# Kernel optimization log

Hardware: AMD Instinct MI355X
Metric: run time of the kernel (lower is better)

## Reference

```python
import jax, jax.numpy as jnp
import numpy as np

N_MELS = 80
FORMANT_START, FORMANT_END = 10, 50
W_L1, W_DELTA, W_DELTA2, W_SC, W_BAND, FORMANT_W = 1.0, 0.5, 0.25, 0.5, 1.0, 2.0
EPS = 1e-8


def _masked_mean(x, mask):
    # mask broadcasts to x's shape; count = sum of the broadcast mask
    n = jnp.maximum(jnp.sum(jnp.broadcast_to(mask, x.shape)), 1.0)
    return jnp.sum(x * mask) / n


def setup_inputs() -> dict:
    key = jax.random.key(0)
    k1, k2, k3 = jax.random.split(key, 3)
    B, T, D = 64, 4000, N_MELS
    pred_mel = jax.random.normal(k1, (B, T, D), dtype=jnp.float32)
    target_mel = jax.random.normal(k2, (B, T, D), dtype=jnp.float32)
    lengths = jax.random.randint(k3, (B,), T // 2, T + 1)
    mel_mask = (jnp.arange(T)[None, :] < lengths[:, None]).astype(jnp.float32)
    band_weights = jnp.ones((D,), dtype=jnp.float32).at[FORMANT_START:FORMANT_END].set(FORMANT_W)
    return {"pred_mel": pred_mel, "target_mel": target_mel, "mel_mask": mel_mask,
            "band_weights": band_weights}


def reference(pred_mel, target_mel, mel_mask, band_weights):
    mask3 = mel_mask[:, :, None]                      # (B,T,1)

    l1 = jnp.abs(pred_mel - target_mel)               # (B,T,D)
    l1_loss = _masked_mean(l1, mask3)

    # 1st-order deltas
    dp = pred_mel[:, 1:] - pred_mel[:, :-1]
    dt = target_mel[:, 1:] - target_mel[:, :-1]
    dmask = (mel_mask[:, 1:] * mel_mask[:, :-1])[:, :, None]
    delta_loss = _masked_mean(jnp.abs(dp - dt), dmask)

    # 2nd-order deltas
    d2p = dp[:, 1:] - dp[:, :-1]
    d2t = dt[:, 1:] - dt[:, :-1]
    d2mask = (mel_mask[:, 2:] * mel_mask[:, 1:-1] * mel_mask[:, :-2])[:, :, None]
    delta2_loss = _masked_mean(jnp.abs(d2p - d2t), d2mask)

    # spectral convergence
    diff = (pred_mel - target_mel) * mask3
    tgt_m = target_mel * mask3
    n = jnp.maximum(jnp.sum(jnp.broadcast_to(mask3, pred_mel.shape)), 1.0)
    sc_num = jnp.sqrt(jnp.sum(diff * diff) / n)
    sc_den = jnp.maximum(jnp.sqrt(jnp.sum(tgt_m * tgt_m) / n), EPS)
    sc_loss = sc_num / sc_den

    # band-weighted L1
    w = band_weights[None, None, :]
    band_loss = _masked_mean(l1 * w, mask3) / jnp.mean(band_weights)

    # energy (per-frame mean over mel bins)
    e_l1 = jnp.abs(pred_mel.mean(axis=-1) - target_mel.mean(axis=-1))  # (B,T)
    energy_loss = _masked_mean(e_l1, mel_mask)

    return (W_L1 * l1_loss + W_DELTA * delta_loss + W_DELTA2 * delta2_loss
            + W_SC * sc_loss + W_BAND * band_loss + 0.5 * energy_loss)
```

## Files before the change

### kernel.cpp

```cpp
#include <hip/hip_runtime.h>
#include <math.h>

#define D_MELS 80
#define T_DIM  4000
#define NQ     10
#define RPB    16
#define NTHR   (RPB * 20)
#define NWAVES (NTHR / 64)
#define NBLK   800


__global__ __launch_bounds__(NTHR) void mel_loss_main(
    const float* __restrict__ pred, const float* __restrict__ tgt,
    const float* __restrict__ mask, const float* __restrict__ w,
    float* __restrict__ ws, int BT)
{
    const int tid = threadIdx.x;
    const int g   = tid % 20;
    const int rl  = tid / 20;

    const float4* p4 = (const float4*)pred;
    const float4* q4 = (const float4*)tgt;
    const float4  wv = ((const float4*)w)[g];

    float v_l1 = 0.f, v_band = 0.f, v_diff2 = 0.f, v_tgt2 = 0.f, v_energy = 0.f;
    float v_m = 0.f, v_d = 0.f, v_dm = 0.f, v_d2 = 0.f, v_d2m = 0.f;

    __shared__ float esum[NTHR];
    __shared__ float red[NWAVES][NQ];

    for (int base = blockIdx.x * RPB; base < BT; base += gridDim.x * RPB) {
        int r = base + rl;
        float my_e = 0.f;
        if (r < BT) {
            int t = r % T_DIM;
            bool has1 = (t >= 1);
            bool has2 = (t >= 2);

            int i0 = r * 20 + g;
            int i1 = has1 ? i0 - 20 : i0;
            int i2 = has2 ? i0 - 40 : i0;

            float4 p  = p4[i0];
            float4 q  = q4[i0];
            float4 pa = p4[i1];
            float4 qa = q4[i1];
            float4 pb = p4[i2];
            float4 qb = q4[i2];

            float mt  = mask[r];
            float mt1 = has1 ? mask[r - 1] : 0.f;
            float mt2 = has2 ? mask[r - 2] : 0.f;

            float e0 = p.x - q.x, e1 = p.y - q.y, e2 = p.z - q.z, e3 = p.w - q.w;
            float f0 = pa.x - qa.x, f1 = pa.y - qa.y, f2 = pa.z - qa.z, f3 = pa.w - qa.w;
            float g0 = pb.x - qb.x, g1 = pb.y - qb.y, g2 = pb.z - qb.z, g3 = pb.w - qb.w;

            float a0 = fabsf(e0), a1 = fabsf(e1), a2 = fabsf(e2), a3 = fabsf(e3);

            float l1r   = a0 + a1 + a2 + a3;
            float bandr = a0 * wv.x + a1 * wv.y + a2 * wv.z + a3 * wv.w;
            float sqr   = e0 * e0 + e1 * e1 + e2 * e2 + e3 * e3;
            float t2r   = q.x * q.x + q.y * q.y + q.z * q.z + q.w * q.w;
            float dr  = fabsf(e0 - f0) + fabsf(e1 - f1) + fabsf(e2 - f2) + fabsf(e3 - f3);
            float d2r = fabsf(e0 - 2.f * f0 + g0) + fabsf(e1 - 2.f * f1 + g1)
                      + fabsf(e2 - 2.f * f2 + g2) + fabsf(e3 - 2.f * f3 + g3);

            float dmv  = mt * mt1;
            float d2mv = mt * mt1 * mt2;

            v_l1    += l1r * mt;
            v_band  += bandr * mt;
            v_diff2 += sqr * mt;
            v_tgt2  += t2r * mt;
            v_d     += dr * dmv;
            v_d2    += d2r * d2mv;
            if (g == 0) {
                v_m   += mt;
                v_dm  += dmv;
                v_d2m += d2mv;
            }
            my_e = e0 + e1 + e2 + e3;
        }
        esum[tid] = my_e;
        __syncthreads();
        if (tid < RPB) {
            int rr = base + tid;
            if (rr < BT) {
                float s = 0.f;
                #pragma unroll
                for (int k = 0; k < 20; ++k) s += esum[tid * 20 + k];
                v_energy += fabsf(s) * mask[rr];
            }
        }
        __syncthreads();
    }

    float vals[NQ] = {v_l1, v_band, v_diff2, v_tgt2, v_energy,
                      v_m, v_d, v_dm, v_d2, v_d2m};
    #pragma unroll
    for (int q = 0; q < NQ; ++q) {
        float v = vals[q];
        #pragma unroll
        for (int off = 32; off > 0; off >>= 1)
            v += __shfl_down(v, off, 64);
        vals[q] = v;
    }

    int wave = tid >> 6;
    int lane = tid & 63;
    if (lane == 0) {
        #pragma unroll
        for (int q = 0; q < NQ; ++q) red[wave][q] = vals[q];
    }
    __syncthreads();
    if (tid < NQ) {
        float s = 0.f;
        #pragma unroll
        for (int wv2 = 0; wv2 < NWAVES; ++wv2) s += red[wv2][tid];
        atomicAdd(&ws[tid], s);
    }
}

__global__ void mel_loss_finalize(const float* __restrict__ ws,
                                  const float* __restrict__ w,
                                  float* __restrict__ out)
{
    if (blockIdx.x == 0 && threadIdx.x == 0) {
        float l1s = ws[0], bands = ws[1], diff2 = ws[2], tgt2 = ws[3];
        float energys = ws[4], ms = ws[5], ds = ws[6], dms = ws[7];
        float d2s = ws[8], d2ms = ws[9];

        float wsum = 0.f;
        for (int d = 0; d < D_MELS; ++d) wsum += w[d];
        float wmean = wsum / (float)D_MELS;

        float n1  = fmaxf(ms  * (float)D_MELS, 1.f);
        float nd  = fmaxf(dms * (float)D_MELS, 1.f);
        float nd2 = fmaxf(d2ms * (float)D_MELS, 1.f);

        float l1_loss     = l1s / n1;
        float delta_loss  = ds / nd;
        float delta2_loss = d2s / nd2;
        float sc_num = sqrtf(diff2 / n1);
        float sc_den = fmaxf(sqrtf(tgt2 / n1), 1e-8f);
        float sc_loss = sc_num / sc_den;
        float band_loss = (bands / n1) / wmean;
        float energy_loss = (energys / (float)D_MELS) / fmaxf(ms, 1.f);

        out[0] = 1.0f * l1_loss + 0.5f * delta_loss + 0.25f * delta2_loss
               + 0.5f * sc_loss + 1.0f * band_loss + 0.5f * energy_loss;
    }
}

extern "C" void kernel_launch(void* const* d_in, const int* in_sizes, int n_in,
                              void* d_out, int out_size, void* d_ws, size_t ws_size,
                              hipStream_t stream) {
    const float* pred = (const float*)d_in[0];
    const float* tgt  = (const float*)d_in[1];
    const float* mask = (const float*)d_in[2];
    const float* w    = (const float*)d_in[3];
    int BT = in_sizes[2];
    float* ws = (float*)d_ws;

    hipMemsetAsync(ws, 0, NQ * sizeof(float), stream);

    mel_loss_main<<<NBLK, NTHR, 0, stream>>>(pred, tgt, mask, w, ws, BT);
    mel_loss_finalize<<<1, 64, 0, stream>>>(ws, w, (float*)d_out);
}
```

Measured before the change: 198.9 us.

## Stage per-tile pred-target differences in LDS with halo for delta terms

```diff
diff --git a/kernel.cpp b/kernel.cpp
--- a/kernel.cpp
+++ b/kernel.cpp
@@ -1,13 +1,17 @@
 #include <hip/hip_runtime.h>
 #include <math.h>
 
-#define D_MELS 80
-#define T_DIM  4000
-#define NQ     10
-#define RPB    16
-#define NTHR   (RPB * 20)
-#define NWAVES (NTHR / 64)
-#define NBLK   800
+#define D_MELS   80
+#define T_DIM    4000
+#define NQ       10
+#define WS_STR   64
+#define NTHR     256
+#define TILE     64
+#define HALO     2
+#define ROWS_LDS (TILE + HALO)
+#define F4_ROW   20
+#define F4_TILE  (ROWS_LDS * F4_ROW)
+#define NBLK     2000
 
 
 __global__ __launch_bounds__(NTHR) void mel_loss_main(
@@ -16,81 +20,91 @@
     float* __restrict__ ws, int BT)
 {
     const int tid = threadIdx.x;
-    const int g   = tid % 20;
-    const int rl  = tid / 20;
-
     const float4* p4 = (const float4*)pred;
     const float4* q4 = (const float4*)tgt;
-    const float4  wv = ((const float4*)w)[g];
+    const float4* w4 = (const float4*)w;
+
+    __shared__ float4 eld[F4_TILE];
+    __shared__ float  msk[ROWS_LDS];
+    __shared__ float  red[NTHR / 64][NQ];
 
     float v_l1 = 0.f, v_band = 0.f, v_diff2 = 0.f, v_tgt2 = 0.f, v_energy = 0.f;
     float v_m = 0.f, v_d = 0.f, v_dm = 0.f, v_d2 = 0.f, v_d2m = 0.f;
 
-    __shared__ float esum[NTHR];
-    __shared__ float red[NWAVES][NQ];
+    for (int base = blockIdx.x * TILE; base < BT; base += gridDim.x * TILE) {
+        if (tid < ROWS_LDS) {
+            int r = base - HALO + tid;
+            msk[tid] = (r >= 0 && r < BT) ? mask[r] : 0.f;
+        }
 
-    for (int base = blockIdx.x * RPB; base < BT; base += gridDim.x * RPB) {
-        int r = base + rl;
-        float my_e = 0.f;
-        if (r < BT) {
-            int t = r % T_DIM;
-            bool has1 = (t >= 1);
-            bool has2 = (t >= 2);
+        #pragma unroll
+        for (int k = 0; k < (F4_TILE + NTHR - 1) / NTHR; ++k) {
+            int f = tid + k * NTHR;
+            if (f < F4_TILE) {
+                int row = base - HALO + f / F4_ROW;
+                float4 e = make_float4(0.f, 0.f, 0.f, 0.f);
+                if (row >= 0 && row < BT) {
+                    int gi = row * F4_ROW + (f % F4_ROW);
+                    float4 p = p4[gi];
+                    float4 q = q4[gi];
+                    e.x = p.x - q.x; e.y = p.y - q.y;
+                    e.z = p.z - q.z; e.w = p.w - q.w;
+                    if (row >= base) {
+                        float mt = mask[row];
+                        float4 wv = w4[f % F4_ROW];
+                        float a0 = fabsf(e.x), a1 = fabsf(e.y),
+                              a2 = fabsf(e.z), a3 = fabsf(e.w);
+                        v_l1    += (a0 + a1 + a2 + a3) * mt;
+                        v_band  += (a0 * wv.x + a1 * wv.y + a2 * wv.z + a3 * wv.w) * mt;
+                        v_diff2 += (e.x * e.x + e.y * e.y + e.z * e.z + e.w * e.w) * mt;
+                        v_tgt2  += (q.x * q.x + q.y * q.y + q.z * q.z + q.w * q.w) * mt;
+                    }
+                }
+                eld[f] = e;
+            }
+        }
+        __syncthreads();
 
-            int i0 = r * 20 + g;
-            int i1 = has1 ? i0 - 20 : i0;
-            int i2 = has2 ? i0 - 40 : i0;
+        {
+            int rl = tid >> 2;
+            int quarter = tid & 3;
+            int r = base + rl;
+            if (r < BT) {
+                int t = r % T_DIM;
+                float m0 = msk[rl + 2];
+                float m1 = (t >= 1) ? msk[rl + 1] : 0.f;
+                float m2 = (t >= 2) ? msk[rl] : 0.f;
+                float dmv  = m0 * m1;
+                float d2mv = dmv * m2;
 
-            float4 p  = p4[i0];
-            float4 q  = q4[i0];
-            float4 pa = p4[i1];
-            float4 qa = q4[i1];
-            float4 pb = p4[i2];
-            float4 qb = q4[i2];
+                const float* ef = (const float*)eld;
+                int off0 = (rl + 2) * D_MELS + quarter * 20;
 
-            float mt  = mask[r];
-            float mt1 = has1 ? mask[r - 1] : 0.f;
-            float mt2 = has2 ? mask[r - 2] : 0.f;
+                float dr = 0.f, d2r = 0.f, er = 0.f;
+                #pragma unroll
+                for (int k = 0; k < 5; ++k) {
+                    float4 e0 = *(const float4*)(ef + off0 + 4 * k);
+                    float4 e1 = *(const float4*)(ef + off0 - D_MELS + 4 * k);
+                    float4 e2 = *(const float4*)(ef + off0 - 2 * D_MELS + 4 * k);
+                    er += e0.x + e0.y + e0.z + e0.w;
+                    dr += fabsf(e0.x - e1.x) + fabsf(e0.y - e1.y)
+                        + fabsf(e0.z - e1.z) + fabsf(e0.w - e1.w);
+                    d2r += fabsf(e0.x - 2.f * e1.x + e2.x)
+                         + fabsf(e0.y - 2.f * e1.y + e2.y)
+                         + fabsf(e0.z - 2.f * e1.z + e2.z)
+                         + fabsf(e0.w - 2.f * e1.w + e2.w);
+                }
+                v_d  += dr * dmv;
+                v_d2 += d2r * d2mv;
 
-            float e0 = p.x - q.x, e1 = p.y - q.y, e2 = p.z - q.z, e3 = p.w - q.w;
-            float f0 = pa.x - qa.x, f1 = pa.y - qa.y, f2 = pa.z - qa.z, f3 = pa.w - qa.w;
-            float g0 = pb.x - qb.x, g1 = pb.y - qb.y, g2 = pb.z - qb.z, g3 = pb.w - qb.w;
-
-            float a0 = fabsf(e0), a1 = fabsf(e1), a2 = fabsf(e2), a3 = fabsf(e3);
-
-            float l1r   = a0 + a1 + a2 + a3;
-            float bandr = a0 * wv.x + a1 * wv.y + a2 * wv.z + a3 * wv.w;
-            float sqr   = e0 * e0 + e1 * e1 + e2 * e2 + e3 * e3;
-            float t2r   = q.x * q.x + q.y * q.y + q.z * q.z + q.w * q.w;
-            float dr  = fabsf(e0 - f0) + fabsf(e1 - f1) + fabsf(e2 - f2) + fabsf(e3 - f3);
-            float d2r = fabsf(e0 - 2.f * f0 + g0) + fabsf(e1 - 2.f * f1 + g1)
-                      + fabsf(e2 - 2.f * f2 + g2) + fabsf(e3 - 2.f * f3 + g3);
-
-            float dmv  = mt * mt1;
-            float d2mv = mt * mt1 * mt2;
-
-            v_l1    += l1r * mt;
-            v_band  += bandr * mt;
-            v_diff2 += sqr * mt;
-            v_tgt2  += t2r * mt;
-            v_d     += dr * dmv;
-            v_d2    += d2r * d2mv;
-            if (g == 0) {
-                v_m   += mt;
-                v_dm  += dmv;
-                v_d2m += d2mv;
-            }
-            my_e = e0 + e1 + e2 + e3;
-        }
-        esum[tid] = my_e;
-        __syncthreads();
-        if (tid < RPB) {
-            int rr = base + tid;
-            if (rr < BT) {
-                float s = 0.f;
-                #pragma unroll
-                for (int k = 0; k < 20; ++k) s += esum[tid * 20 + k];
-                v_energy += fabsf(s) * mask[rr];
+                er += __shfl_xor(er, 1, 64);
+                er += __shfl_xor(er, 2, 64);
+                if (quarter == 0) {
+                    v_energy += fabsf(er) * m0;
+                    v_m   += m0;
+                    v_dm  += dmv;
+                    v_d2m += d2mv;
+                }
             }
         }
         __syncthreads();
@@ -106,9 +120,7 @@
             v += __shfl_down(v, off, 64);
         vals[q] = v;
     }
-
-    int wave = tid >> 6;
-    int lane = tid & 63;
+    int wave = tid >> 6, lane = tid & 63;
     if (lane == 0) {
         #pragma unroll
         for (int q = 0; q < NQ; ++q) red[wave][q] = vals[q];
@@ -117,8 +129,8 @@
     if (tid < NQ) {
         float s = 0.f;
         #pragma unroll
-        for (int wv2 = 0; wv2 < NWAVES; ++wv2) s += red[wv2][tid];
-        atomicAdd(&ws[tid], s);
+        for (int wv = 0; wv < NTHR / 64; ++wv) s += red[wv][tid];
+        atomicAdd(&ws[tid * WS_STR], s);
     }
 }
 
@@ -127,16 +139,18 @@
                                   float* __restrict__ out)
 {
     if (blockIdx.x == 0 && threadIdx.x == 0) {
-        float l1s = ws[0], bands = ws[1], diff2 = ws[2], tgt2 = ws[3];
-        float energys = ws[4], ms = ws[5], ds = ws[6], dms = ws[7];
-        float d2s = ws[8], d2ms = ws[9];
+        float l1s   = ws[0 * WS_STR], bands = ws[1 * WS_STR];
+        float diff2 = ws[2 * WS_STR], tgt2  = ws[3 * WS_STR];
+        float energys = ws[4 * WS_STR], ms  = ws[5 * WS_STR];
+        float ds    = ws[6 * WS_STR], dms   = ws[7 * WS_STR];
+        float d2s   = ws[8 * WS_STR], d2ms  = ws[9 * WS_STR];
 
         float wsum = 0.f;
         for (int d = 0; d < D_MELS; ++d) wsum += w[d];
         float wmean = wsum / (float)D_MELS;
 
-        float n1  = fmaxf(ms  * (float)D_MELS, 1.f);
-        float nd  = fmaxf(dms * (float)D_MELS, 1.f);
+        float n1  = fmaxf(ms   * (float)D_MELS, 1.f);
+        float nd  = fmaxf(dms  * (float)D_MELS, 1.f);
         float nd2 = fmaxf(d2ms * (float)D_MELS, 1.f);
 
         float l1_loss     = l1s / n1;
@@ -163,8 +177,10 @@
     int BT = in_sizes[2];
     float* ws = (float*)d_ws;
 
-    hipMemsetAsync(ws, 0, NQ * sizeof(float), stream);
+    hipMemsetAsync(ws, 0, NQ * WS_STR * sizeof(float), stream);
 
-    mel_loss_main<<<NBLK, NTHR, 0, stream>>>(pred, tgt, mask, w, ws, BT);
+    int tiles = (BT + TILE - 1) / TILE;
+    int grid = tiles < NBLK ? tiles : NBLK;
+    mel_loss_main<<<grid, NTHR, 0, stream>>>(pred, tgt, mask, w, ws, BT);
     mel_loss_finalize<<<1, 64, 0, stream>>>(ws, w, (float*)d_out);
 }
```

Measured after the change: 207.2 us. 4.2% more time.

## Map 16 rows per wave with 4 lanes per row, drop block syncs and atomics

Applied to the files above, without the earlier changes.

```diff
diff --git a/kernel.cpp b/kernel.cpp
--- a/kernel.cpp
+++ b/kernel.cpp
@@ -1,73 +1,90 @@
 #include <hip/hip_runtime.h>
 #include <math.h>
 
-#define D_MELS 80
-#define T_DIM  4000
-#define NQ     10
-#define RPB    16
-#define NTHR   (RPB * 20)
-#define NWAVES (NTHR / 64)
-#define NBLK   800
+#define D_MELS  80
+#define T_DIM   4000
+#define F4_ROW  20
+#define NQ      10
+#define NTHR    256
+#define MAXB    1024
 
 
 __global__ __launch_bounds__(NTHR) void mel_loss_main(
     const float* __restrict__ pred, const float* __restrict__ tgt,
     const float* __restrict__ mask, const float* __restrict__ w,
-    float* __restrict__ ws, int BT)
+    float* __restrict__ partial, int BT, int nwaves_total)
 {
-    const int tid = threadIdx.x;
-    const int g   = tid % 20;
-    const int rl  = tid / 20;
+    const int tid  = threadIdx.x;
+    const int lane = tid & 63;
+    const int qtr  = lane & 3;
+    const int rw   = lane >> 2;
+    const int gwave = blockIdx.x * (NTHR / 64) + (tid >> 6);
 
     const float4* p4 = (const float4*)pred;
     const float4* q4 = (const float4*)tgt;
-    const float4  wv = ((const float4*)w)[g];
+
+    float4 wv[5];
+    #pragma unroll
+    for (int k = 0; k < 5; ++k) wv[k] = ((const float4*)w)[qtr + 4 * k];
 
     float v_l1 = 0.f, v_band = 0.f, v_diff2 = 0.f, v_tgt2 = 0.f, v_energy = 0.f;
     float v_m = 0.f, v_d = 0.f, v_dm = 0.f, v_d2 = 0.f, v_d2m = 0.f;
 
-    __shared__ float esum[NTHR];
-    __shared__ float red[NWAVES][NQ];
+    const int row_stride = nwaves_total * 16;
 
-    for (int base = blockIdx.x * RPB; base < BT; base += gridDim.x * RPB) {
-        int r = base + rl;
-        float my_e = 0.f;
+    for (int rbase = gwave * 16; rbase < BT; rbase += row_stride) {
+        int r = rbase + rw;
         if (r < BT) {
             int t = r % T_DIM;
             bool has1 = (t >= 1);
             bool has2 = (t >= 2);
 
-            int i0 = r * 20 + g;
-            int i1 = has1 ? i0 - 20 : i0;
-            int i2 = has2 ? i0 - 40 : i0;
-
-            float4 p  = p4[i0];
-            float4 q  = q4[i0];
-            float4 pa = p4[i1];
-            float4 qa = q4[i1];
-            float4 pb = p4[i2];
-            float4 qb = q4[i2];
+            const float4* pr0 = p4 + (size_t)r * F4_ROW + qtr;
+            const float4* qr0 = q4 + (size_t)r * F4_ROW + qtr;
+            const float4* pr1 = has1 ? pr0 - F4_ROW : pr0;
+            const float4* qr1 = has1 ? qr0 - F4_ROW : qr0;
+            const float4* pr2 = has2 ? pr0 - 2 * F4_ROW : pr0;
+            const float4* qr2 = has2 ? qr0 - 2 * F4_ROW : qr0;
 
             float mt  = mask[r];
             float mt1 = has1 ? mask[r - 1] : 0.f;
             float mt2 = has2 ? mask[r - 2] : 0.f;
 
-            float e0 = p.x - q.x, e1 = p.y - q.y, e2 = p.z - q.z, e3 = p.w - q.w;
-            float f0 = pa.x - qa.x, f1 = pa.y - qa.y, f2 = pa.z - qa.z, f3 = pa.w - qa.w;
-            float g0 = pb.x - qb.x, g1 = pb.y - qb.y, g2 = pb.z - qb.z, g3 = pb.w - qb.w;
+            float l1r = 0.f, bandr = 0.f, sqr = 0.f, t2r = 0.f, er = 0.f;
+            float dr = 0.f, d2r = 0.f;
 
-            float a0 = fabsf(e0), a1 = fabsf(e1), a2 = fabsf(e2), a3 = fabsf(e3);
+            #pragma unroll
+            for (int k = 0; k < 5; ++k) {
+                float4 p  = pr0[4 * k];
+                float4 qq = qr0[4 * k];
+                float4 pa = pr1[4 * k];
+                float4 qa = qr1[4 * k];
+                float4 pb = pr2[4 * k];
+                float4 qb = qr2[4 * k];
 
-            float l1r   = a0 + a1 + a2 + a3;
-            float bandr = a0 * wv.x + a1 * wv.y + a2 * wv.z + a3 * wv.w;
-            float sqr   = e0 * e0 + e1 * e1 + e2 * e2 + e3 * e3;
-            float t2r   = q.x * q.x + q.y * q.y + q.z * q.z + q.w * q.w;
-            float dr  = fabsf(e0 - f0) + fabsf(e1 - f1) + fabsf(e2 - f2) + fabsf(e3 - f3);
-            float d2r = fabsf(e0 - 2.f * f0 + g0) + fabsf(e1 - 2.f * f1 + g1)
-                      + fabsf(e2 - 2.f * f2 + g2) + fabsf(e3 - 2.f * f3 + g3);
+                float e0 = p.x - qq.x, e1 = p.y - qq.y,
+                      e2 = p.z - qq.z, e3 = p.w - qq.w;
+                float f0 = pa.x - qa.x, f1 = pa.y - qa.y,
+                      f2 = pa.z - qa.z, f3 = pa.w - qa.w;
+                float g0 = pb.x - qb.x, g1 = pb.y - qb.y,
+                      g2 = pb.z - qb.z, g3 = pb.w - qb.w;
+
+                float a0 = fabsf(e0), a1 = fabsf(e1),
+                      a2 = fabsf(e2), a3 = fabsf(e3);
+
+                l1r   += a0 + a1 + a2 + a3;
+                bandr += a0 * wv[k].x + a1 * wv[k].y + a2 * wv[k].z + a3 * wv[k].w;
+                sqr   += e0 * e0 + e1 * e1 + e2 * e2 + e3 * e3;
+                t2r   += qq.x * qq.x + qq.y * qq.y + qq.z * qq.z + qq.w * qq.w;
+                er    += e0 + e1 + e2 + e3;
+                dr  += fabsf(e0 - f0) + fabsf(e1 - f1)
+                     + fabsf(e2 - f2) + fabsf(e3 - f3);
+                d2r += fabsf(e0 - 2.f * f0 + g0) + fabsf(e1 - 2.f * f1 + g1)
+                     + fabsf(e2 - 2.f * f2 + g2) + fabsf(e3 - 2.f * f3 + g3);
+            }
 
             float dmv  = mt * mt1;
-            float d2mv = mt * mt1 * mt2;
+            float d2mv = dmv * mt2;
 
             v_l1    += l1r * mt;
             v_band  += bandr * mt;
@@ -75,25 +92,16 @@
             v_tgt2  += t2r * mt;
             v_d     += dr * dmv;
             v_d2    += d2r * d2mv;
-            if (g == 0) {
+
+            er += __shfl_xor(er, 1, 64);
+            er += __shfl_xor(er, 2, 64);
+            if (qtr == 0) {
+                v_energy += fabsf(er) * mt;
                 v_m   += mt;
                 v_dm  += dmv;
                 v_d2m += d2mv;
             }
-            my_e = e0 + e1 + e2 + e3;
         }
-        esum[tid] = my_e;
-        __syncthreads();
-        if (tid < RPB) {
-            int rr = base + tid;
-            if (rr < BT) {
-                float s = 0.f;
-                #pragma unroll
-                for (int k = 0; k < 20; ++k) s += esum[tid * 20 + k];
-                v_energy += fabsf(s) * mask[rr];
-            }
-        }
-        __syncthreads();
     }
 
     float vals[NQ] = {v_l1, v_band, v_diff2, v_tgt2, v_energy,
@@ -106,9 +114,8 @@
             v += __shfl_down(v, off, 64);
         vals[q] = v;
     }
-
+    __shared__ float red[NTHR / 64][NQ];
     int wave = tid >> 6;
-    int lane = tid & 63;
     if (lane == 0) {
         #pragma unroll
         for (int q = 0; q < NQ; ++q) red[wave][q] = vals[q];
@@ -117,26 +124,38 @@
     if (tid < NQ) {
         float s = 0.f;
         #pragma unroll
-        for (int wv2 = 0; wv2 < NWAVES; ++wv2) s += red[wv2][tid];
-        atomicAdd(&ws[tid], s);
+        for (int wv2 = 0; wv2 < NTHR / 64; ++wv2) s += red[wv2][tid];
+        partial[tid * MAXB + blockIdx.x] = s;
     }
 }
 
-__global__ void mel_loss_finalize(const float* __restrict__ ws,
-                                  const float* __restrict__ w,
-                                  float* __restrict__ out)
+__global__ __launch_bounds__(640) void mel_loss_finalize(
+    const float* __restrict__ partial, const float* __restrict__ w,
+    float* __restrict__ out, int nblk)
 {
-    if (blockIdx.x == 0 && threadIdx.x == 0) {
-        float l1s = ws[0], bands = ws[1], diff2 = ws[2], tgt2 = ws[3];
-        float energys = ws[4], ms = ws[5], ds = ws[6], dms = ws[7];
-        float d2s = ws[8], d2ms = ws[9];
+    const int tid = threadIdx.x;
+    const int wv  = tid >> 6;
+    const int lane = tid & 63;
+    __shared__ float fin[NQ];
+
+    float s = 0.f;
+    for (int i = lane; i < nblk; i += 64) s += partial[wv * MAXB + i];
+    #pragma unroll
+    for (int off = 32; off > 0; off >>= 1) s += __shfl_down(s, off, 64);
+    if (lane == 0) fin[wv] = s;
+    __syncthreads();
+
+    if (tid == 0) {
+        float l1s = fin[0], bands = fin[1], diff2 = fin[2], tgt2 = fin[3];
+        float energys = fin[4], ms = fin[5], ds = fin[6], dms = fin[7];
+        float d2s = fin[8], d2ms = fin[9];
 
         float wsum = 0.f;
         for (int d = 0; d < D_MELS; ++d) wsum += w[d];
         float wmean = wsum / (float)D_MELS;
 
-        float n1  = fmaxf(ms  * (float)D_MELS, 1.f);
-        float nd  = fmaxf(dms * (float)D_MELS, 1.f);
+        float n1  = fmaxf(ms   * (float)D_MELS, 1.f);
+        float nd  = fmaxf(dms  * (float)D_MELS, 1.f);
         float nd2 = fmaxf(d2ms * (float)D_MELS, 1.f);
 
         float l1_loss     = l1s / n1;
@@ -161,10 +180,13 @@
     const float* mask = (const float*)d_in[2];
     const float* w    = (const float*)d_in[3];
     int BT = in_sizes[2];
-    float* ws = (float*)d_ws;
+    float* partial = (float*)d_ws;
 
-    hipMemsetAsync(ws, 0, NQ * sizeof(float), stream);
+    int rows_per_block = (NTHR / 64) * 16;
+    int blocks_needed = (BT + rows_per_block - 1) / rows_per_block;
+    int grid = blocks_needed < MAXB ? blocks_needed : MAXB;
+    int nwaves_total = grid * (NTHR / 64);
 
-    mel_loss_main<<<NBLK, NTHR, 0, stream>>>(pred, tgt, mask, w, ws, BT);
-    mel_loss_finalize<<<1, 64, 0, stream>>>(ws, w, (float*)d_out);
+    mel_loss_main<<<grid, NTHR, 0, stream>>>(pred, tgt, mask, w, partial, BT, nwaves_total);
+    mel_loss_finalize<<<1, 640, 0, stream>>>(partial, w, (float*)d_out, grid);
 }
```

After: 193.4 us. -2.8%, faster.
